# Performance work log

Measured on AMD Instinct MI355X. Metric: run time of the kernel, lower is better.

## Reference

```python
import jax, jax.numpy as jnp
import numpy as np

B, T, V = 128, 400, 148
E, ENC, DEC, NM, A, H = 512, 512, 1024, 80, 128, 256

def conv1d(x, w, pad):
    # x: [B,C_in,L], w: [C_out,C_in,K]
    return jax.lax.conv_general_dilated(x, w, (1,), [(pad, pad)],
                                        dimension_numbers=('NCH', 'OIH', 'NCH'))

def setup_inputs() -> dict:
    key = jax.random.key(0)
    ks = jax.random.split(key, 40)
    rn = lambda k, shp, s: jax.random.normal(k, shp, jnp.float32) * s
    inp = {
        'text': jax.random.randint(ks[0], (B, T), 0, V, jnp.int32),
        'mels': rn(ks[1], (B, NM, T), 1.0),
        'emb': rn(ks[2], (V, E), 0.3),
        'enc_conv_w': rn(ks[3], (ENC, E, 5), 0.02), 'enc_conv_b': jnp.zeros((ENC,)),
        'bn_g': jnp.ones((ENC,)), 'bn_b': jnp.zeros((ENC,)),
        'lstm_Wih': rn(ks[4], (3, 2, 4 * H, ENC), 0.04),
        'lstm_Whh': rn(ks[5], (3, 2, 4 * H, H), 0.06),
        'lstm_b': jnp.zeros((3, 2, 4 * H)),
        'pre_W1': rn(ks[6], (256, NM), 0.1), 'pre_b1': jnp.zeros((256,)),
        'pre_W2': rn(ks[7], (256, 256), 0.06), 'pre_b2': jnp.zeros((256,)),
        'att_Wq': rn(ks[8], (A, DEC), 0.03), 'att_Wm': rn(ks[9], (A, ENC), 0.04),
        'att_Wloc': rn(ks[10], (A, 2, 31), 0.1), 'att_v': rn(ks[11], (A,), 1.0),
        'dec_Wih': rn(ks[12], (4 * DEC, 256 + ENC), 0.03),
        'dec_Whh': rn(ks[13], (4 * DEC, DEC), 0.03),
        'dec_b': jnp.zeros((4 * DEC,)),
        'out_W': rn(ks[14], (NM * 3, DEC + ENC), 0.025), 'out_b': jnp.zeros((NM * 3,)),
        'post_w1': rn(ks[15], (512, NM, 5), 0.05), 'post_b1': jnp.zeros((512,)),
        'post_g': jnp.ones((512,)), 'post_bta': jnp.zeros((512,)),
        'post_w2': rn(ks[16], (NM, 512, 5), 0.02), 'post_b2': jnp.zeros((NM,)),
    }
    return inp

def reference(text, mels, emb, enc_conv_w, enc_conv_b, bn_g, bn_b,
              lstm_Wih, lstm_Whh, lstm_b, pre_W1, pre_b1, pre_W2, pre_b2,
              att_Wq, att_Wm, att_Wloc, att_v, dec_Wih, dec_Whh, dec_b,
              out_W, out_b, post_w1, post_b1, post_g, post_bta, post_w2, post_b2):
    b, t = text.shape
    n_mels = mels.shape[1]
    # --- encoder ---
    x = emb[text].transpose(0, 2, 1)                        # [B,E,T]
    x = jax.nn.relu(conv1d(x, enc_conv_w, 2) + enc_conv_b[None, :, None])
    mu = x.mean(axis=(0, 2), keepdims=True)
    var = x.var(axis=(0, 2), keepdims=True)                 # BatchNorm1d, train mode
    x = (x - mu) / jnp.sqrt(var + 1e-5) * bn_g[None, :, None] + bn_b[None, :, None]
    h = x.transpose(2, 0, 1)                                # [T,B,ENC] time-major

    def lstm_scan(seq, Wih, Whh, bb, rev):
        def step(carry, xt):
            hh, cc = carry
            g = xt @ Wih.T + hh @ Whh.T + bb
            i, f, gg, o = jnp.split(g, 4, axis=-1)
            cc = jax.nn.sigmoid(f) * cc + jax.nn.sigmoid(i) * jnp.tanh(gg)
            hh = jax.nn.sigmoid(o) * jnp.tanh(cc)
            return (hh, cc), hh
        z = jnp.zeros((seq.shape[1], Whh.shape[-1]), seq.dtype)
        _, hs = jax.lax.scan(step, (z, z), seq, reverse=rev)
        return hs

    for l in range(3):                                      # 3-layer biLSTM
        fwd = lstm_scan(h, lstm_Wih[l, 0], lstm_Whh[l, 0], lstm_b[l, 0], False)
        bwd = lstm_scan(h, lstm_Wih[l, 1], lstm_Whh[l, 1], lstm_b[l, 1], True)
        h = jnp.concatenate([fwd, bwd], axis=-1)            # [T,B,ENC]
    memory = h.transpose(1, 0, 2)                           # [B,T,ENC]
    pm = memory @ att_Wm.T                                  # [B,T,A] (constant over steps)
    mels_tm = mels.transpose(2, 0, 1)                       # [T,B,NM] teacher forcing
    D = dec_Whh.shape[-1]

    def dec_step(carry, mel_t):
        dec_in, hd, cd, cum = carry                         # cum: [B,2,T]
        pre = jax.nn.relu(jax.nn.relu(dec_in @ pre_W1.T + pre_b1) @ pre_W2.T + pre_b2)
        pl = conv1d(cum, att_Wloc, 15)                      # [B,A,T]
        pq = hd @ att_Wq.T                                  # [B,A]
        e = jnp.tanh(pq[:, None, :] + pm + pl.transpose(0, 2, 1)) @ att_v  # [B,T]
        align = jax.nn.softmax(e, axis=-1)
        ctx = jnp.einsum('bt,btd->bd', align, memory)       # [B,ENC]
        cum = cum + align[:, None, :]
        g = jnp.concatenate([pre, ctx], -1) @ dec_Wih.T + hd @ dec_Whh.T + dec_b
        i, f, gg, o = jnp.split(g, 4, axis=-1)
        cd = jax.nn.sigmoid(f) * cd + jax.nn.sigmoid(i) * jnp.tanh(gg)
        hd = jax.nn.sigmoid(o) * jnp.tanh(cd)
        mo = (jnp.concatenate([hd, ctx], -1) @ out_W.T + out_b).reshape(-1, 3, n_mels)
        gate = jax.nn.sigmoid(mo[:, :, -1])                 # [B,3]
        return (mel_t, hd, cd, cum), (mo, gate)

    dt = mels.dtype
    carry0 = (jnp.zeros((b, n_mels), dt), jnp.zeros((b, D), dt),
              jnp.zeros((b, D), dt), jnp.zeros((b, 2, t), dt))
    _, (mos, gates) = jax.lax.scan(dec_step, carry0, mels_tm)
    mel_outputs = mos.transpose(1, 0, 2, 3).reshape(b, 3 * t, n_mels).transpose(0, 2, 1)  # [B,NM,3T]
    gate_outputs = gates.transpose(1, 0, 2).reshape(b, 3 * t)
    # --- postnet ---
    p = conv1d(mel_outputs, post_w1, 2) + post_b1[None, :, None]
    mu = p.mean(axis=(0, 2), keepdims=True)
    var = p.var(axis=(0, 2), keepdims=True)
    p = (p - mu) / jnp.sqrt(var + 1e-5) * post_g[None, :, None] + post_bta[None, :, None]
    p = conv1d(jnp.tanh(p), post_w2, 2) + post_b2[None, :, None]
    mel_postnet = p + mel_outputs
    return mel_outputs, mel_postnet, gate_outputs
```

## Files before the change

### kernel.cpp

```cpp
#include <hip/hip_runtime.h>
#include <hip/hip_fp16.h>
#include <cstdio>
#include <cstddef>

typedef unsigned short u16;
typedef unsigned int u32;

#define BB   128
#define TT   400
#define EE   512
#define HH   256
#define NMEL 80
#define AA   128
#define DD   1024
#define T3   1200
#define PRESPLIT 352

__device__ __forceinline__ float b2f(u16 h) { return __uint_as_float(((u32)h) << 16); }
__device__ __forceinline__ u16 f2b(float f) {
    u32 x = __float_as_uint(f);
    u32 r = (x + 0x7FFFu + ((x >> 16) & 1u)) >> 16;
    return (u16)r;
}
__device__ __forceinline__ float sigm(float x) { return 1.0f / (1.0f + __expf(-x)); }

template<int F32> __device__ __forceinline__ float ldf(const void* p, size_t i) {
    if (F32) return ((const float*)p)[i];
    return b2f(((const u16*)p)[i]);
}
template<int F32> __device__ __forceinline__ float4 ldf4(const void* p, size_t i) {
    if (F32) return *(const float4*)((const float*)p + i);
    ushort4 w = *(const ushort4*)((const u16*)p + i);
    return make_float4(b2f(w.x), b2f(w.y), b2f(w.z), b2f(w.w));
}
template<int F32> __device__ __forceinline__ void stf(void* p, size_t i, float v) {
    if (F32) ((float*)p)[i] = v;
    else ((u16*)p)[i] = f2b(v);
}

__global__ __launch_bounds__(256) void k_detect(const void* emb, int* flag) {
    int tid = threadIdx.x;
    const u16* p = (const u16*)emb;
    int insane = 0;
    for (int i = tid; i < 4096; i += 256) {
        u16 h = p[2 * i];
        u32 ex = (h >> 7) & 0xFF;
        if (ex < 96 || ex > 159) insane++;
    }
    __shared__ int red[256];
    red[tid] = insane; __syncthreads();
    for (int st = 128; st > 0; st >>= 1) {
        if (tid < st) red[tid] += red[tid + st];
        __syncthreads();
    }
    if (tid == 0) *flag = (red[0] > 1024) ? 1 : 0;
}

template<int F32> __device__ __forceinline__ void embed_body(const int* text, const void* emb, float* X) {
    int e = blockIdx.x, b = blockIdx.y;
    for (int t = threadIdx.x; t < TT; t += 256) {
        int v = text[b * TT + t];
        X[((size_t)b * EE + e) * TT + t] = ldf<F32>(emb, (size_t)v * EE + e);
    }
}
__global__ __launch_bounds__(256) void k_embed(const int* text, const void* emb, float* X, const int* flag) {
    if (*flag) embed_body<1>(text, emb, X); else embed_body<0>(text, emb, X);
}

template<int F32> __device__ __forceinline__
void encconv_body(const float* X, const void* W, const void* bias, float* Y, float* xs) {
    int t0 = blockIdx.x * 64, o0 = blockIdx.y * 32, b = blockIdx.z;
    int tid = threadIdx.x;
    int ol = tid >> 3, tg = tid & 7;
    int o = o0 + ol, tl = tg * 8;
    float acc[8];
    float bv = ldf<F32>(bias, o);
    #pragma unroll
    for (int j = 0; j < 8; ++j) acc[j] = bv;
    for (int q = 0; q < 4; ++q) {
        __syncthreads();
        for (int idx = tid; idx < 128 * 68; idx += 256) {
            int il = idx / 68, rest = idx - il * 68;
            int t = t0 - 2 + rest;
            float v = 0.f;
            if (t >= 0 && t < TT) v = X[((size_t)b * EE + q * 128 + il) * TT + t];
            xs[idx] = v;
        }
        __syncthreads();
        size_t wbase = ((size_t)o * EE + q * 128) * 5;
        for (int il = 0; il < 128; ++il) {
            float xv[12];
            #pragma unroll
            for (int j = 0; j < 12; ++j) xv[j] = xs[il * 68 + tl + j];
            #pragma unroll
            for (int k = 0; k < 5; ++k) {
                float w = ldf<F32>(W, wbase + il * 5 + k);
                #pragma unroll
                for (int j = 0; j < 8; ++j) acc[j] += w * xv[j + k];
            }
        }
    }
    #pragma unroll
    for (int j = 0; j < 8; ++j) {
        int t = t0 + tl + j;
        if (t < TT) Y[((size_t)b * EE + o) * TT + t] = acc[j] > 0.f ? acc[j] : 0.f;
    }
}
__global__ __launch_bounds__(256) void k_encconv(const float* X, const void* W, const void* bias, float* Y, const int* flag) {
    __shared__ float xs[128 * 68];
    if (*flag) encconv_body<1>(X, W, bias, Y, xs); else encconv_body<0>(X, W, bias, Y, xs);
}

template<int INF32> __device__ __forceinline__
void bnstats_body(const void* Y, float* mu, float* rs, int L, int C, int Bn) {
    int o = blockIdx.x, tid = threadIdx.x;
    float s = 0.f, s2 = 0.f;
    for (int b = 0; b < Bn; ++b) {
        size_t base = ((size_t)b * C + o) * L;
        for (int t = tid; t < L; t += 256) {
            float v = INF32 ? ((const float*)Y)[base + t] : b2f(((const u16*)Y)[base + t]);
            s += v; s2 += v * v;
        }
    }
    __shared__ float r1[256], r2[256];
    r1[tid] = s; r2[tid] = s2; __syncthreads();
    for (int st = 128; st > 0; st >>= 1) {
        if (tid < st) { r1[tid] += r1[tid + st]; r2[tid] += r2[tid + st]; }
        __syncthreads();
    }
    if (tid == 0) {
        float n = (float)Bn * (float)L;
        float m = r1[0] / n;
        float var = r2[0] / n - m * m;
        mu[o] = m;
        rs[o] = 1.0f / sqrtf(var + 1e-5f);
    }
}
__global__ __launch_bounds__(256) void k_bnstats(const void* Y, float* mu, float* rs, int L, int C, int Bn, int inf32) {
    if (inf32) bnstats_body<1>(Y, mu, rs, L, C, Bn); else bnstats_body<0>(Y, mu, rs, L, C, Bn);
}

template<int F32> __device__ __forceinline__
void bnapply_body(const float* Y, const float* mu, const float* rs, const void* g, const void* beta,
                  float* H, float* tile) {
    int t0 = blockIdx.x * 64, c0 = blockIdx.y * 64, b = blockIdx.z;
    int tid = threadIdx.x;
    for (int idx = tid; idx < 64 * 64; idx += 256) {
        int cl = idx >> 6, tl = idx & 63;
        int t = t0 + tl, c = c0 + cl;
        float v = 0.f;
        if (t < TT) v = Y[((size_t)b * EE + c) * TT + t];
        tile[cl * 65 + tl] = (v - mu[c]) * rs[c] * ldf<F32>(g, c) + ldf<F32>(beta, c);
    }
    __syncthreads();
    for (int idx = tid; idx < 64 * 64; idx += 256) {
        int tl = idx >> 6, cl = idx & 63;
        int t = t0 + tl;
        if (t < TT) H[((size_t)t * BB + b) * EE + c0 + cl] = tile[cl * 65 + tl];
    }
}
__global__ __launch_bounds__(256) void k_bnapply(const float* Y, const float* mu, const float* rs,
                                                 const void* g, const void* beta, float* H, const int* flag) {
    __shared__ float tile[64 * 65];
    if (*flag) bnapply_body<1>(Y, mu, rs, g, beta, H, tile); else bnapply_body<0>(Y, mu, rs, g, beta, H, tile);
}

template<int F32> __device__ __forceinline__
void transEnc_body(const void* Wih, const void* Whh, float* WtE) {
    int ld = blockIdx.x;
    int k  = blockIdx.y;
    int u  = threadIdx.x;
    float4 w;
    if (k < 512) {
        size_t base = (size_t)ld * 1024 * 512;
        w.x = ldf<F32>(Wih, base + (size_t)(u)       * 512 + k);
        w.y = ldf<F32>(Wih, base + (size_t)(256 + u) * 512 + k);
        w.z = ldf<F32>(Wih, base + (size_t)(512 + u) * 512 + k);
        w.w = ldf<F32>(Wih, base + (size_t)(768 + u) * 512 + k);
    } else {
        size_t base = (size_t)ld * 1024 * 256;
        int kk = k - 512;
        w.x = ldf<F32>(Whh, base + (size_t)(u)       * 256 + kk);
        w.y = ldf<F32>(Whh, base + (size_t)(256 + u) * 256 + kk);
        w.z = ldf<F32>(Whh, base + (size_t)(512 + u) * 256 + kk);
        w.w = ldf<F32>(Whh, base + (size_t)(768 + u) * 256 + kk);
    }
    ((float4*)WtE)[((size_t)ld * 768 + k) * 256 + u] = w;
}
__global__ __launch_bounds__(256) void k_transEnc(const void* Wih, const void* Whh, float* WtE, const int* flag) {
    if (*flag) transEnc_body<1>(Wih, Whh, WtE); else transEnc_body<0>(Wih, Whh, WtE);
}

template<int F32> __device__ __forceinline__
void lstm2_body(const float* Hin, float* Hout, const float* WtE, const void* b_all, int layer,
                float* xsh, float* hsh) {
    int d = blockIdx.x >> 6;
    int b0 = (blockIdx.x & 63) * 2;
    int u = threadIdx.x;
    int ld = layer * 2 + d;
    size_t bB = (size_t)ld * 1024;
    float bi_ = ldf<F32>(b_all, bB + u),       bf_ = ldf<F32>(b_all, bB + 256 + u);
    float bg_ = ldf<F32>(b_all, bB + 512 + u), bo_ = ldf<F32>(b_all, bB + 768 + u);
    const float4* W4 = (const float4*)WtE + (size_t)ld * 768 * 256 + u;
    float c0v = 0.f, c1v = 0.f;
    hsh[u] = 0.f; hsh[256 + u] = 0.f;
    for (int s = 0; s < TT; ++s) {
        int t = d ? (TT - 1 - s) : s;
        __syncthreads();
        const float* src = Hin + ((size_t)t * BB + b0) * EE;
        xsh[u] = src[u];             xsh[256 + u] = src[256 + u];
        xsh[512 + u] = src[512 + u]; xsh[768 + u] = src[768 + u];
        __syncthreads();
        float a0i = bi_, a0f = bf_, a0g = bg_, a0o = bo_;
        float a1i = bi_, a1f = bf_, a1g = bg_, a1o = bo_;
        #pragma unroll 8
        for (int k = 0; k < 512; ++k) {
            float4 w = W4[(size_t)k * 256];
            float x0 = xsh[k], x1 = xsh[512 + k];
            a0i += w.x * x0; a0f += w.y * x0; a0g += w.z * x0; a0o += w.w * x0;
            a1i += w.x * x1; a1f += w.y * x1; a1g += w.z * x1; a1o += w.w * x1;
        }
        #pragma unroll 8
        for (int k = 0; k < 256; ++k) {
            float4 w = W4[(size_t)(512 + k) * 256];
            float h0 = hsh[k], h1 = hsh[256 + k];
            a0i += w.x * h0; a0f += w.y * h0; a0g += w.z * h0; a0o += w.w * h0;
            a1i += w.x * h1; a1f += w.y * h1; a1g += w.z * h1; a1o += w.w * h1;
        }
        float i0 = sigm(a0i), f0 = sigm(a0f), g0 = tanhf(a0g), o0v = sigm(a0o);
        c0v = f0 * c0v + i0 * g0;
        float h0v = o0v * tanhf(c0v);
        float i1 = sigm(a1i), f1 = sigm(a1f), g1 = tanhf(a1g), o1v = sigm(a1o);
        c1v = f1 * c1v + i1 * g1;
        float h1v = o1v * tanhf(c1v);
        __syncthreads();
        hsh[u] = h0v; hsh[256 + u] = h1v;
        Hout[((size_t)t * BB + b0) * EE + d * HH + u]     = h0v;
        Hout[((size_t)t * BB + b0 + 1) * EE + d * HH + u] = h1v;
    }
}
__global__ __launch_bounds__(256) void k_lstm2(const float* Hin, float* Hout, const float* WtE,
                                               const void* bb, int layer, const int* flag) {
    __shared__ __align__(16) float xsh[1024];
    __shared__ __align__(16) float hsh[512];
    if (*flag) lstm2_body<1>(Hin, Hout, WtE, bb, layer, xsh, hsh);
    else       lstm2_body<0>(Hin, Hout, WtE, bb, layer, xsh, hsh);
}

template<int F32> __device__ __forceinline__
void pm_body(const float* H1, const void* Wm, float* PM, float* xsh) {
    int t0 = blockIdx.x * 8, b = blockIdx.y;
    int tid = threadIdx.x;
    for (int idx = tid; idx < 8 * 512; idx += 128) {
        int tt = idx >> 9, k = idx & 511;
        xsh[tt * 512 + k] = H1[((size_t)(t0 + tt) * BB + b) * EE + k];
    }
    __syncthreads();
    size_t wrow = (size_t)tid * 512;
    float acc[8] = {0, 0, 0, 0, 0, 0, 0, 0};
    for (int k = 0; k < 512; k += 4) {
        float4 w = ldf4<F32>(Wm, wrow + k);
        #pragma unroll
        for (int tt = 0; tt < 8; ++tt) {
            float4 x = *(const float4*)&xsh[tt * 512 + k];
            acc[tt] += w.x * x.x; acc[tt] += w.y * x.y; acc[tt] += w.z * x.z; acc[tt] += w.w * x.w;
        }
    }
    #pragma unroll
    for (int tt = 0; tt < 8; ++tt)
        PM[((size_t)(t0 + tt) * BB + b) * AA + tid] = acc[tt];
}
__global__ __launch_bounds__(128) void k_pm(const float* H1, const void* Wm, float* PM, const int* flag) {
    __shared__ __align__(16) float xsh[8 * 512];
    if (*flag) pm_body<1>(H1, Wm, PM, xsh); else pm_body<0>(H1, Wm, PM, xsh);
}

template<int F32> __device__ __forceinline__
void transPre_body(const void* W1, const void* W2, float* W1t, float* W2t) {
    int r = blockIdx.x, j = threadIdx.x;
    if (r < 80) W1t[r * 256 + j] = ldf<F32>(W1, (size_t)j * 80 + r);
    else { int k = r - 80; W2t[k * 256 + j] = ldf<F32>(W2, (size_t)j * 256 + k); }
}
__global__ __launch_bounds__(256) void k_transPre(const void* W1, const void* W2, float* W1t, float* W2t, const int* flag) {
    if (*flag) transPre_body<1>(W1, W2, W1t, W2t); else transPre_body<0>(W1, W2, W1t, W2t);
}

template<int F32> __device__ __forceinline__
void prenet_all_body(const void* mels, const float* W1t, const float* W2t, const void* b1, const void* b2,
                     float* PREm, float* PREt, float* melsh, float* h1sh) {
    int t0 = blockIdx.x * 16, b = blockIdx.y;
    int tid = threadIdx.x;
    for (int idx = tid; idx < 16 * 80; idx += 256) {
        int tl = idx / 80, m = idx - tl * 80;
        int t = t0 + tl;
        melsh[tl * 80 + m] = (t == 0) ? 0.f : ldf<F32>(mels, ((size_t)b * NMEL + m) * TT + (t - 1));
    }
    __syncthreads();
    {
        int j = tid;
        float acc[16];
        float bv = ldf<F32>(b1, j);
        #pragma unroll
        for (int tl = 0; tl < 16; ++tl) acc[tl] = bv;
        for (int m = 0; m < 80; ++m) {
            float w = W1t[m * 256 + j];
            #pragma unroll
            for (int tl = 0; tl < 16; ++tl) acc[tl] += w * melsh[tl * 80 + m];
        }
        #pragma unroll
        for (int tl = 0; tl < 16; ++tl) h1sh[tl * 256 + j] = acc[tl] > 0.f ? acc[tl] : 0.f;
    }
    __syncthreads();
    {
        int j = tid;
        float acc[16];
        float bv = ldf<F32>(b2, j);
        #pragma unroll
        for (int tl = 0; tl < 16; ++tl) acc[tl] = bv;
        for (int k = 0; k < 256; ++k) {
            float w = W2t[k * 256 + j];
            #pragma unroll
            for (int tl = 0; tl < 16; ++tl) acc[tl] += w * h1sh[tl * 256 + k];
        }
        #pragma unroll
        for (int tl = 0; tl < 16; ++tl) {
            float v = acc[tl] > 0.f ? acc[tl] : 0.f;
            size_t ix = ((size_t)(t0 + tl) * BB + b) * HH + j;
            if (t0 < PRESPLIT) PREm[ix] = v;
            else               PREt[ix - (size_t)PRESPLIT * BB * HH] = v;
        }
    }
}
__global__ __launch_bounds__(256) void k_prenet_all(const void* mels, const float* W1t, const float* W2t,
                                                    const void* b1, const void* b2,
                                                    float* PREm, float* PREt, const int* flag) {
    __shared__ float melsh[16 * 80];
    __shared__ float h1sh[16 * 256];
    if (*flag) prenet_all_body<1>(mels, W1t, W2t, b1, b2, PREm, PREt, melsh, h1sh);
    else       prenet_all_body<0>(mels, W1t, W2t, b1, b2, PREm, PREt, melsh, h1sh);
}

__global__ void k_weff(const void* Wloc, float* weff, const int* flag) {
    int a = threadIdx.x;
    if (*flag) {
        for (int k = 0; k < 31; ++k)
            weff[a * 31 + k] = ldf<1>(Wloc, (size_t)(a * 2) * 31 + k) + ldf<1>(Wloc, (size_t)(a * 2 + 1) * 31 + k);
    } else {
        for (int k = 0; k < 31; ++k)
            weff[a * 31 + k] = ldf<0>(Wloc, (size_t)(a * 2) * 31 + k) + ldf<0>(Wloc, (size_t)(a * 2 + 1) * 31 + k);
    }
}

template<int F32> __device__ __forceinline__
void transW_body(const void* Wih, const void* Whh, float* Wt2) {
    int u = blockIdx.x * 256 + threadIdx.x;
    int k = blockIdx.y;
    float4 w;
    if (k < 768) {
        w.x = ldf<F32>(Wih, (size_t)(0 * 1024 + u) * 768 + k);
        w.y = ldf<F32>(Wih, (size_t)(1 * 1024 + u) * 768 + k);
        w.z = ldf<F32>(Wih, (size_t)(2 * 1024 + u) * 768 + k);
        w.w = ldf<F32>(Wih, (size_t)(3 * 1024 + u) * 768 + k);
    } else {
        int kk = k - 768;
        w.x = ldf<F32>(Whh, (size_t)(0 * 1024 + u) * 1024 + kk);
        w.y = ldf<F32>(Whh, (size_t)(1 * 1024 + u) * 1024 + kk);
        w.z = ldf<F32>(Whh, (size_t)(2 * 1024 + u) * 1024 + kk);
        w.w = ldf<F32>(Whh, (size_t)(3 * 1024 + u) * 1024 + kk);
    }
    ((float4*)Wt2)[(size_t)k * 1024 + u] = w;
}
__global__ __launch_bounds__(256) void k_transW(const void* Wih, const void* Whh, float* Wt2, const int* flag) {
    if (*flag) transW_body<1>(Wih, Whh, Wt2); else transW_body<0>(Wih, Whh, Wt2);
}

__global__ __launch_bounds__(256) void k_transOut(const void* outW, float* outWt, const int* flag) {
    int k = blockIdx.x;
    int j = threadIdx.x;
    if (j < 240) {
        float v = (*flag) ? ldf<1>(outW, (size_t)j * 1536 + k) : ldf<0>(outW, (size_t)j * 1536 + k);
        outWt[(size_t)k * 240 + j] = v;
    }
}
__global__ __launch_bounds__(128) void k_transWq(const void* Wq, float* Wqt, const int* flag) {
    int k = blockIdx.x;
    int a = threadIdx.x;
    float v = (*flag) ? ldf<1>(Wq, (size_t)a * 1024 + k) : ldf<0>(Wq, (size_t)a * 1024 + k);
    Wqt[(size_t)k * AA + a] = v;
}

template<int F32> __device__ __forceinline__
void att_body(int b, const float* hin, const float* ctxp, float* ctxc,
              const float* Wqt, const float* PM, float* cum, const float* weff,
              const void* att_v, const float* outWt, const void* outB, void* dout,
              const float* H1, int t,
              float* xsh, float* opart, float* pqsh, float* cpad, float* al, float* part, float* red)
{
    int tid = threadIdx.x;
    xsh[tid]       = hin[(size_t)b * DD + tid];
    xsh[512 + tid] = hin[(size_t)b * DD + 512 + tid];
    if (t > 0) xsh[1024 + (tid & 511)] = ctxp[(size_t)b * EE + (tid & 511)];
    for (int i = tid; i < 432; i += 512) {
        int pos = i - 15;
        cpad[i] = (pos >= 0 && pos < TT) ? cum[b * TT + pos] : 0.f;
    }
    __syncthreads();

    if (t > 0) {
        int j = -1, half = 0;
        if (tid < 240) { j = tid; half = 0; }
        else if (tid >= 256 && tid < 496) { j = tid - 256; half = 1; }
        if (j >= 0) {
            const float* wp = outWt + (half ? (size_t)768 * 240 : 0);
            const float* xp = xsh + (half ? 768 : 0);
            float a0 = 0, a1 = 0, a2 = 0, a3 = 0;
            for (int k = 0; k < 768; k += 4) {
                a0 += wp[(size_t)(k + 0) * 240 + j] * xp[k + 0];
                a1 += wp[(size_t)(k + 1) * 240 + j] * xp[k + 1];
                a2 += wp[(size_t)(k + 2) * 240 + j] * xp[k + 2];
                a3 += wp[(size_t)(k + 3) * 240 + j] * xp[k + 3];
            }
            opart[half * 240 + j] = (a0 + a1) + (a2 + a3);
        }
        __syncthreads();
        if (tid < 240) {
            float acc = ldf<F32>(outB, tid) + opart[tid] + opart[240 + tid];
            int jj = tid / 80, mm = tid - jj * 80;
            int col = 3 * (t - 1) + jj;
            stf<F32>(dout, (size_t)b * 96000 + (size_t)mm * 1200 + col, acc);
            if (mm == 79) stf<F32>(dout, (size_t)24576000 + (size_t)b * 1200 + col, sigm(acc));
        }
    }

    {
        int a = tid & 127, q = tid >> 7;
        float acc = 0.f;
        const float* wq = Wqt + a;
        int k0 = q * 256;
        for (int k = k0; k < k0 + 256; k += 4) {
            acc += wq[(size_t)(k + 0) * AA] * xsh[k + 0];
            acc += wq[(size_t)(k + 1) * AA] * xsh[k + 1];
            acc += wq[(size_t)(k + 2) * AA] * xsh[k + 2];
            acc += wq[(size_t)(k + 3) * AA] * xsh[k + 3];
        }
        pqsh[q * 128 + a] = acc;
    }
    __syncthreads();

    {
        int a = tid & 127, q = tid >> 7;
        float pqv = pqsh[a] + pqsh[128 + a] + pqsh[256 + a] + pqsh[384 + a];
        float vv = ldf<F32>(att_v, a);
        float wr[31];
        #pragma unroll
        for (int k = 0; k < 31; ++k) wr[k] = weff[a * 31 + k];
        int lane = tid & 63;
        int wid2 = (tid >> 6) & 1;
        for (int tt = q; tt < TT; tt += 4) {
            float acc = pqv + PM[((size_t)tt * BB + b) * AA + a];
            #pragma unroll
            for (int k = 0; k < 31; ++k) acc += wr[k] * cpad[tt + k];
            float fv = tanhf(acc) * vv;
            #pragma unroll
            for (int m = 1; m < 64; m <<= 1) fv += __shfl_xor(fv, m, 64);
            if (lane == 0) part[tt * 2 + wid2] = fv;
        }
    }
    __syncthreads();

    float mx = -1e30f;
    for (int tt = tid; tt < TT; tt += 512) { float v = part[2 * tt] + part[2 * tt + 1]; al[tt] = v; mx = fmaxf(mx, v); }
    red[tid] = mx; __syncthreads();
    for (int st = 256; st > 0; st >>= 1) { if (tid < st) red[tid] = fmaxf(red[tid], red[tid + st]); __syncthreads(); }
    mx = red[0]; __syncthreads();
    float s = 0.f;
    for (int tt = tid; tt < TT; tt += 512) { float v = __expf(al[tt] - mx); al[tt] = v; s += v; }
    red[tid] = s; __syncthreads();
    for (int st = 256; st > 0; st >>= 1) { if (tid < st) red[tid] += red[tid + st]; __syncthreads(); }
    float inv = 1.0f / red[0];
    __syncthreads();
    for (int tt = tid; tt < TT; tt += 512) { float v = al[tt] * inv; al[tt] = v; cum[b * TT + tt] += v; }
    __syncthreads();

    {
        int d = tid;
        float a0 = 0, a1 = 0, a2 = 0, a3 = 0;
        for (int tt = 0; tt < TT; tt += 4) {
            a0 += al[tt + 0] * H1[((size_t)(tt + 0) * BB + b) * EE + d];
            a1 += al[tt + 1] * H1[((size_t)(tt + 1) * BB + b) * EE + d];
            a2 += al[tt + 2] * H1[((size_t)(tt + 2) * BB + b) * EE + d];
            a3 += al[tt + 3] * H1[((size_t)(tt + 3) * BB + b) * EE + d];
        }
        ctxc[(size_t)b * EE + d] = (a0 + a1) + (a2 + a3);
    }
}

__device__ __forceinline__
void gemm_hd_body(int bid, const float* hin, const float* Wt2, float* gpart, float* xs) {
    int bt = bid >> 4, ut = bid & 15;
    int b0 = bt * 8, u0 = ut * 64;
    int tid = threadIdx.x;
    int u_l = tid & 63, bq = tid >> 6;
    int u = u0 + u_l;
    for (int idx = tid; idx < 1024 * 8; idx += 512) {
        int b_l = idx >> 10, kl = idx & 1023;
        xs[kl * 9 + b_l] = hin[(size_t)(b0 + b_l) * DD + kl];
    }
    __syncthreads();
    float ai = 0.f, af = 0.f, ag = 0.f, ao = 0.f;
    const float4* wp = (const float4*)Wt2 + (size_t)768 * 1024 + u;
    #pragma unroll 8
    for (int kl = 0; kl < 1024; ++kl) {
        float4 w = wp[(size_t)kl * 1024];
        float x = xs[kl * 9 + bq];
        ai += w.x * x; af += w.y * x; ag += w.z * x; ao += w.w * x;
    }
    ((float4*)gpart)[(size_t)(b0 + bq) * 1024 + u] = make_float4(ai, af, ag, ao);
}

__global__ __launch_bounds__(512) void k_att_gemm(const float* hin, const float* ctxp, float* ctxc,
                                                  const float* Wqt, const float* PM, float* cum, const float* weff,
                                                  const void* att_v, const float* outWt, const void* outB, void* dout,
                                                  const float* H1, const float* Wt2, float* gpart,
                                                  int t, const int* flag) {
    __shared__ __align__(16) float smem[9216];
    if (blockIdx.x < 128) {
        int b = blockIdx.x;
        float* xsh   = smem;
        float* opart = smem + 1536;
        float* pqsh  = smem + 2016;
        float* cpad  = smem + 2528;
        float* al    = smem + 2960;
        float* part  = smem + 3360;
        float* red   = smem + 4160;
        if (*flag) att_body<1>(b, hin, ctxp, ctxc, Wqt, PM, cum, weff, att_v, outWt, outB, dout, H1, t,
                               xsh, opart, pqsh, cpad, al, part, red);
        else       att_body<0>(b, hin, ctxp, ctxc, Wqt, PM, cum, weff, att_v, outWt, outB, dout, H1, t,
                               xsh, opart, pqsh, cpad, al, part, red);
    } else {
        gemm_hd_body(blockIdx.x - 128, hin, Wt2, gpart, smem);
    }
}

__global__ __launch_bounds__(512) void k_dec_lstm3(const float* PREm, const float* PREt,
                                                   const float* ctx, const float* Wt2, const void* bbp,
                                                   const float* gpart, float* hd_out, float* cd,
                                                   int t, const int* flag) {
    __shared__ float xs[768 * 9];
    int bt = blockIdx.x >> 4, ut = blockIdx.x & 15;
    int b0 = bt * 8, u0 = ut * 64;
    int tid = threadIdx.x;
    int u_l = tid & 63, bq = tid >> 6;
    int u = u0 + u_l, b = b0 + bq;
    int f32 = *flag;
    const float* prep = (t < PRESPLIT) ? (PREm + (size_t)t * BB * HH)
                                       : (PREt + (size_t)(t - PRESPLIT) * BB * HH);
    float ai, af, ag, ao;
    if (f32) {
        ai = ldf<1>(bbp, u);        af = ldf<1>(bbp, u + 1024);
        ag = ldf<1>(bbp, u + 2048); ao = ldf<1>(bbp, u + 3072);
    } else {
        ai = ldf<0>(bbp, u);        af = ldf<0>(bbp, u + 1024);
        ag = ldf<0>(bbp, u + 2048); ao = ldf<0>(bbp, u + 3072);
    }
    for (int idx = tid; idx < 768 * 8; idx += 512) {
        int b_l = idx / 768, kl = idx - b_l * 768;
        int bb_ = b0 + b_l;
        float v = (kl < 256) ? prep[(size_t)bb_ * HH + kl] : ctx[(size_t)bb_ * EE + (kl - 256)];
        xs[kl * 9 + b_l] = v;
    }
    __syncthreads();
    const float4* wp = (const float4*)Wt2 + u;
    #pragma unroll 8
    for (int kl = 0; kl < 768; ++kl) {
        float4 w = wp[(size_t)kl * 1024];
        float x = xs[kl * 9 + bq];
        ai += w.x * x; af += w.y * x; ag += w.z * x; ao += w.w * x;
    }
    float4 gp = ((const float4*)gpart)[(size_t)b * 1024 + u];
    ai += gp.x; af += gp.y; ag += gp.z; ao += gp.w;
    float iv = sigm(ai), fv = sigm(af), gv = tanhf(ag), ov = sigm(ao);
    float c = cd[(size_t)b * DD + u];
    c = fv * c + iv * gv;
    cd[(size_t)b * DD + u] = c;
    hd_out[(size_t)b * DD + u] = ov * tanhf(c);
}

template<int F32> __device__ __forceinline__
void dec_out_body(const float* hd, const float* ctx, const float* outWt, const void* outB,
                  void* dout, int t, float* xsh) {
    int b = blockIdx.x, tid = threadIdx.x;
    for (int idx = tid; idx < 1536; idx += 256)
        xsh[idx] = (idx < 1024) ? hd[(size_t)b * DD + idx] : ctx[(size_t)b * EE + (idx - 1024)];
    __syncthreads();
    if (tid < 240) {
        float a0 = 0, a1 = 0, a2 = 0, a3 = 0;
        for (int k = 0; k < 1536; k += 4) {
            a0 += outWt[(size_t)(k + 0) * 240 + tid] * xsh[k + 0];
            a1 += outWt[(size_t)(k + 1) * 240 + tid] * xsh[k + 1];
            a2 += outWt[(size_t)(k + 2) * 240 + tid] * xsh[k + 2];
            a3 += outWt[(size_t)(k + 3) * 240 + tid] * xsh[k + 3];
        }
        float acc = ldf<F32>(outB, tid) + ((a0 + a1) + (a2 + a3));
        int j = tid / 80, mm = tid - j * 80;
        int col = 3 * t + j;
        stf<F32>(dout, (size_t)b * 96000 + (size_t)mm * 1200 + col, acc);
        if (mm == 79) stf<F32>(dout, (size_t)24576000 + (size_t)b * 1200 + col, sigm(acc));
    }
}
__global__ __launch_bounds__(256) void k_dec_out2(const float* hd, const float* ctx, const float* outWt,
                                                  const void* outB, void* dout, int t, const int* flag) {
    __shared__ __align__(16) float xsh[1536];
    if (*flag) dec_out_body<1>(hd, ctx, outWt, outB, dout, t, xsh);
    else       dec_out_body<0>(hd, ctx, outWt, outB, dout, t, xsh);
}

template<int F32> __device__ __forceinline__
void post1_body(const void* dout, const void* W, const void* bias, u16* P1, u16* msh) {
    int t0 = blockIdx.x * 64, o0 = blockIdx.y * 32, b = blockIdx.z;
    int tid = threadIdx.x;
    for (int idx = tid; idx < 80 * 68; idx += 256) {
        int i = idx / 68, rest = idx - i * 68;
        int t = t0 - 2 + rest;
        u16 v = 0;
        if (t >= 0 && t < T3) v = f2b(ldf<F32>(dout, (size_t)b * 96000 + (size_t)i * 1200 + t));
        msh[idx] = v;
    }
    __syncthreads();
    int ol = tid >> 3, tg = tid & 7;
    int o = o0 + ol, tl = tg * 8;
    float acc[8];
    float bv = ldf<F32>(bias, o);
    #pragma unroll
    for (int j = 0; j < 8; ++j) acc[j] = bv;
    size_t wrow = (size_t)o * 400;
    for (int i = 0; i < 80; ++i) {
        float xv[12];
        #pragma unroll
        for (int j = 0; j < 12; ++j) xv[j] = b2f(msh[i * 68 + tl + j]);
        #pragma unroll
        for (int k = 0; k < 5; ++k) {
            float w = ldf<F32>(W, wrow + i * 5 + k);
            #pragma unroll
            for (int j = 0; j < 8; ++j) acc[j] += w * xv[j + k];
        }
    }
    #pragma unroll
    for (int j = 0; j < 8; ++j) {
        int t = t0 + tl + j;
        if (t < T3) P1[((size_t)b * EE + o) * T3 + t] = f2b(acc[j]);
    }
}
__global__ __launch_bounds__(256) void k_post1(const void* dout, const void* W, const void* bias,
                                               u16* P1, const int* flag) {
    __shared__ u16 msh[80 * 68];
    if (*flag) post1_body<1>(dout, W, bias, P1, msh); else post1_body<0>(dout, W, bias, P1, msh);
}

template<int F32> __device__ __forceinline__
void post2_body(const u16* P1, const float* mu, const float* rs, const void* g, const void* beta,
                const void* W2, const void* b2v, void* dout, float* tsh) {
    int t0 = blockIdx.x * 32, b = blockIdx.y;
    int tid = threadIdx.x;
    int tl = tid >> 3, mg = tid & 7;
    float acc[10];
    #pragma unroll
    for (int q = 0; q < 10; ++q) acc[q] = ldf<F32>(b2v, mg + 8 * q);
    for (int oc = 0; oc < 4; ++oc) {
        int o0 = oc * 128;
        __syncthreads();
        for (int idx = tid; idx < 128 * 36; idx += 256) {
            int i = idx / 36, rest = idx - i * 36;
            int t = t0 - 2 + rest;
            float v = 0.f;
            if (t >= 0 && t < T3) {
                int o = o0 + i;
                float raw = b2f(P1[((size_t)b * EE + o) * T3 + t]);
                v = tanhf((raw - mu[o]) * rs[o] * ldf<F32>(g, o) + ldf<F32>(beta, o));
            }
            tsh[i * 37 + rest] = v;
        }
        __syncthreads();
        for (int i = 0; i < 128; ++i) {
            float xv[5];
            #pragma unroll
            for (int k = 0; k < 5; ++k) xv[k] = tsh[i * 37 + tl + k];
            #pragma unroll
            for (int q = 0; q < 10; ++q) {
                int m = mg + 8 * q;
                size_t wp = ((size_t)m * 512 + o0 + i) * 5;
                acc[q] += ldf<F32>(W2, wp + 0) * xv[0];
                acc[q] += ldf<F32>(W2, wp + 1) * xv[1];
                acc[q] += ldf<F32>(W2, wp + 2) * xv[2];
                acc[q] += ldf<F32>(W2, wp + 3) * xv[3];
                acc[q] += ldf<F32>(W2, wp + 4) * xv[4];
            }
        }
    }
    int t = t0 + tl;
    if (t < T3) {
        #pragma unroll
        for (int q = 0; q < 10; ++q) {
            int m = mg + 8 * q;
            size_t idx = (size_t)b * 96000 + (size_t)m * 1200 + t;
            float res = ldf<F32>(dout, idx);
            stf<F32>(dout, (size_t)12288000 + idx, acc[q] + res);
        }
    }
}
__global__ __launch_bounds__(256) void k_post2(const u16* P1, const float* mu, const float* rs,
                                               const void* g, const void* beta, const void* W2,
                                               const void* b2v, void* dout, const int* flag) {
    __shared__ float tsh[128 * 37];
    if (*flag) post2_body<1>(P1, mu, rs, g, beta, W2, b2v, dout, tsh);
    else       post2_body<0>(P1, mu, rs, g, beta, W2, b2v, dout, tsh);
}

extern "C" void kernel_launch(void* const* d_in, const int* in_sizes, int n_in,
                              void* d_out, int out_size, void* d_ws, size_t ws_size,
                              hipStream_t stream) {
    const int*  text       = (const int*)d_in[0];
    const void* mels       = d_in[1];
    const void* emb        = d_in[2];
    const void* enc_conv_w = d_in[3];
    const void* enc_conv_b = d_in[4];
    const void* bn_g       = d_in[5];
    const void* bn_b       = d_in[6];
    const void* lstm_Wih   = d_in[7];
    const void* lstm_Whh   = d_in[8];
    const void* lstm_b     = d_in[9];
    const void* pre_W1     = d_in[10];
    const void* pre_b1     = d_in[11];
    const void* pre_W2     = d_in[12];
    const void* pre_b2     = d_in[13];
    const void* att_Wq     = d_in[14];
    const void* att_Wm     = d_in[15];
    const void* att_Wloc   = d_in[16];
    const void* att_v      = d_in[17];
    const void* dec_Wih    = d_in[18];
    const void* dec_Whh    = d_in[19];
    const void* dec_b      = d_in[20];
    const void* out_W      = d_in[21];
    const void* out_b      = d_in[22];
    const void* post_w1    = d_in[23];
    const void* post_b1    = d_in[24];
    const void* post_g     = d_in[25];
    const void* post_bta   = d_in[26];
    const void* post_w2    = d_in[27];
    const void* post_b2    = d_in[28];

    const size_t WS_NEED = 212049924;
    if (ws_size < WS_NEED) {
        fprintf(stderr, "kernel_launch: ws_size %zu < needed %zu\n", ws_size, WS_NEED);
        return;
    }
    char* ws = (char*)d_ws;
    float* X    = (float*)(ws + 0);
    float* Yf   = (float*)(ws + 104857600);
    float* H0f  = (float*)(ws + 0);
    float* Af   = (float*)(ws + 104857600);
    float* Bf   = (float*)(ws + 0);
    float* H1f  = (float*)(ws + 104857600);
    float* PM    = (float*)(ws + 0);
    float* Wt2   = (float*)(ws + 26214400);
    float* outWt = (float*)(ws + 55574528);
    float* Wqt   = (float*)(ws + 57049088);
    float* W1t   = (float*)(ws + 57573376);
    float* W2t   = (float*)(ws + 57655296);
    float* PREm  = (float*)(ws + 57917440);
    float* PREt  = (float*)d_out + 12288000;
    float* gpart = (float*)d_out + 14000000;
    u16*   P1    = (u16*)(ws + 0);
    float* WtE   = (float*)d_out;
    char* SM = ws + 209715200;
    float* weff  = (float*)(SM + 0);
    float* encmu = (float*)(SM + 16384);
    float* encrs = (float*)(SM + 18432);
    float* pmu   = (float*)(SM + 20480);
    float* prs   = (float*)(SM + 22528);
    float* cum   = (float*)(SM + 24576);
    float* ctx0  = (float*)(SM + 229376);
    float* ctx1  = (float*)(SM + 491520);
    float* hd0   = (float*)(SM + 753664);
    float* hd1   = (float*)(SM + 1277952);
    float* cd    = (float*)(SM + 1802240);
    int*   flag  = (int*)(SM + 2326528);

    k_detect<<<1, 256, 0, stream>>>(emb, flag);
    hipMemsetAsync(SM, 0, 2326528, stream);
    k_weff<<<1, 128, 0, stream>>>(att_Wloc, weff, flag);
    k_transEnc<<<dim3(6, 768), 256, 0, stream>>>(lstm_Wih, lstm_Whh, WtE, flag);

    k_embed<<<dim3(512, 128), 256, 0, stream>>>(text, emb, X, flag);
    k_encconv<<<dim3(7, 16, 128), 256, 0, stream>>>(X, enc_conv_w, enc_conv_b, Yf, flag);
    k_bnstats<<<512, 256, 0, stream>>>(Yf, encmu, encrs, 400, 512, 128, 1);
    k_bnapply<<<dim3(7, 8, 128), 256, 0, stream>>>(Yf, encmu, encrs, bn_g, bn_b, H0f, flag);
    k_lstm2<<<128, 256, 0, stream>>>(H0f, Af, WtE, lstm_b, 0, flag);
    k_lstm2<<<128, 256, 0, stream>>>(Af, Bf, WtE, lstm_b, 1, flag);
    k_lstm2<<<128, 256, 0, stream>>>(Bf, H1f, WtE, lstm_b, 2, flag);

    k_transW<<<dim3(4, 1792), 256, 0, stream>>>(dec_Wih, dec_Whh, Wt2, flag);
    k_transOut<<<1536, 256, 0, stream>>>(out_W, outWt, flag);
    k_transWq<<<1024, 128, 0, stream>>>(att_Wq, Wqt, flag);
    k_transPre<<<336, 256, 0, stream>>>(pre_W1, pre_W2, W1t, W2t, flag);
    k_pm<<<dim3(50, 128), 128, 0, stream>>>(H1f, att_Wm, PM, flag);
    k_prenet_all<<<dim3(25, 128), 256, 0, stream>>>(mels, W1t, W2t, pre_b1, pre_b2, PREm, PREt, flag);

    for (int t = 0; t < TT; ++t) {
        float* hin  = (t & 1) ? hd1 : hd0;
        float* hout = (t & 1) ? hd0 : hd1;
        float* ctxp = (t & 1) ? ctx0 : ctx1;
        float* ctxc = (t & 1) ? ctx1 : ctx0;
        k_att_gemm<<<384, 512, 0, stream>>>(hin, ctxp, ctxc, Wqt, PM, cum, weff, att_v,
                                            outWt, out_b, d_out, H1f, Wt2, gpart, t, flag);
        k_dec_lstm3<<<256, 512, 0, stream>>>(PREm, PREt, ctxc, Wt2, dec_b, gpart, hout, cd, t, flag);
    }
    k_dec_out2<<<128, 256, 0, stream>>>(hd0, ctx1, outWt, out_b, d_out, TT - 1, flag);

    k_post1<<<dim3(19, 16, 128), 256, 0, stream>>>(d_out, post_w1, post_b1, P1, flag);
    k_bnstats<<<512, 256, 0, stream>>>(P1, pmu, prs, 1200, 512, 128, 0);
    k_post2<<<dim3(38, 128), 256, 0, stream>>>(P1, pmu, prs, post_g, post_bta, post_w2, post_b2, d_out, flag);
}
```

Baseline: 141.5 ms.

## Retile decoder LSTM GEMMs to 64-batch x 16-unit blocks with k-slabs

```diff
diff --git a/kernel.cpp b/kernel.cpp
--- a/kernel.cpp
+++ b/kernel.cpp
@@ -497,25 +497,34 @@
 
 __device__ __forceinline__
 void gemm_hd_body(int bid, const float* hin, const float* Wt2, float* gpart, float* xs) {
-    int bt = bid >> 4, ut = bid & 15;
-    int b0 = bt * 8, u0 = ut * 64;
-    int tid = threadIdx.x;
-    int u_l = tid & 63, bq = tid >> 6;
+    int bt = bid >> 6, ut = bid & 63;
+    int b0 = bt * 64, u0 = ut * 16;
+    int tid = threadIdx.x;
+    int u_l = tid & 15, bl = tid >> 4;
     int u = u0 + u_l;
-    for (int idx = tid; idx < 1024 * 8; idx += 512) {
-        int b_l = idx >> 10, kl = idx & 1023;
-        xs[kl * 9 + b_l] = hin[(size_t)(b0 + b_l) * DD + kl];
-    }
-    __syncthreads();
-    float ai = 0.f, af = 0.f, ag = 0.f, ao = 0.f;
-    const float4* wp = (const float4*)Wt2 + (size_t)768 * 1024 + u;
-    #pragma unroll 8
-    for (int kl = 0; kl < 1024; ++kl) {
-        float4 w = wp[(size_t)kl * 1024];
-        float x = xs[kl * 9 + bq];
-        ai += w.x * x; af += w.y * x; ag += w.z * x; ao += w.w * x;
-    }
-    ((float4*)gpart)[(size_t)(b0 + bq) * 1024 + u] = make_float4(ai, af, ag, ao);
+    int b_a = 2 * bl, b_b = 2 * bl + 1;
+    float ai0 = 0, af0 = 0, ag0 = 0, ao0 = 0;
+    float ai1 = 0, af1 = 0, ag1 = 0, ao1 = 0;
+    for (int slab = 0; slab < 8; ++slab) {
+        int k0 = slab * 128;
+        __syncthreads();
+        for (int idx = tid; idx < 8192; idx += 512) {
+            int b_l = idx >> 7, kk = idx & 127;
+            xs[kk * 65 + b_l] = hin[(size_t)(b0 + b_l) * DD + k0 + kk];
+        }
+        __syncthreads();
+        const float4* wp = (const float4*)Wt2 + (size_t)(768 + k0) * 1024 + u;
+        #pragma unroll 4
+        for (int kk = 0; kk < 128; ++kk) {
+            float4 w = wp[(size_t)kk * 1024];
+            float x0 = xs[kk * 65 + b_a];
+            float x1 = xs[kk * 65 + b_b];
+            ai0 += w.x * x0; af0 += w.y * x0; ag0 += w.z * x0; ao0 += w.w * x0;
+            ai1 += w.x * x1; af1 += w.y * x1; ag1 += w.z * x1; ao1 += w.w * x1;
+        }
+    }
+    ((float4*)gpart)[(size_t)(b0 + b_a) * 1024 + u] = make_float4(ai0, af0, ag0, ao0);
+    ((float4*)gpart)[(size_t)(b0 + b_b) * 1024 + u] = make_float4(ai1, af1, ag1, ao1);
 }
 
 __global__ __launch_bounds__(512) void k_att_gemm(const float* hin, const float* ctxp, float* ctxc,
@@ -523,7 +532,7 @@
                                                   const void* att_v, const float* outWt, const void* outB, void* dout,
                                                   const float* H1, const float* Wt2, float* gpart,
                                                   int t, const int* flag) {
-    __shared__ __align__(16) float smem[9216];
+    __shared__ __align__(16) float smem[128 * 65];
     if (blockIdx.x < 128) {
         int b = blockIdx.x;
         float* xsh   = smem;
@@ -546,44 +555,65 @@
                                                    const float* ctx, const float* Wt2, const void* bbp,
                                                    const float* gpart, float* hd_out, float* cd,
                                                    int t, const int* flag) {
-    __shared__ float xs[768 * 9];
-    int bt = blockIdx.x >> 4, ut = blockIdx.x & 15;
-    int b0 = bt * 8, u0 = ut * 64;
-    int tid = threadIdx.x;
-    int u_l = tid & 63, bq = tid >> 6;
-    int u = u0 + u_l, b = b0 + bq;
+    __shared__ __align__(16) float xs[128 * 65];
+    int bt = blockIdx.x >> 6, ut = blockIdx.x & 63;
+    int b0 = bt * 64, u0 = ut * 16;
+    int tid = threadIdx.x;
+    int u_l = tid & 15, bl = tid >> 4;
+    int u = u0 + u_l;
+    int b_a = b0 + 2 * bl, b_b = b0 + 2 * bl + 1;
     int f32 = *flag;
     const float* prep = (t < PRESPLIT) ? (PREm + (size_t)t * BB * HH)
                                        : (PREt + (size_t)(t - PRESPLIT) * BB * HH);
-    float ai, af, ag, ao;
+    float bi, bf_, bg, bo;
     if (f32) {
-        ai = ldf<1>(bbp, u);        af = ldf<1>(bbp, u + 1024);
-        ag = ldf<1>(bbp, u + 2048); ao = ldf<1>(bbp, u + 3072);
+        bi = ldf<1>(bbp, u);        bf_ = ldf<1>(bbp, u + 1024);
+        bg = ldf<1>(bbp, u + 2048); bo  = ldf<1>(bbp, u + 3072);
     } else {
-        ai = ldf<0>(bbp, u);        af = ldf<0>(bbp, u + 1024);
-        ag = ldf<0>(bbp, u + 2048); ao = ldf<0>(bbp, u + 3072);
-    }
-    for (int idx = tid; idx < 768 * 8; idx += 512) {
-        int b_l = idx / 768, kl = idx - b_l * 768;
-        int bb_ = b0 + b_l;
-        float v = (kl < 256) ? prep[(size_t)bb_ * HH + kl] : ctx[(size_t)bb_ * EE + (kl - 256)];
-        xs[kl * 9 + b_l] = v;
-    }
-    __syncthreads();
-    const float4* wp = (const float4*)Wt2 + u;
-    #pragma unroll 8
-    for (int kl = 0; kl < 768; ++kl) {
-        float4 w = wp[(size_t)kl * 1024];
-        float x = xs[kl * 9 + bq];
-        ai += w.x * x; af += w.y * x; ag += w.z * x; ao += w.w * x;
-    }
-    float4 gp = ((const float4*)gpart)[(size_t)b * 1024 + u];
-    ai += gp.x; af += gp.y; ag += gp.z; ao += gp.w;
-    float iv = sigm(ai), fv = sigm(af), gv = tanhf(ag), ov = sigm(ao);
-    float c = cd[(size_t)b * DD + u];
-    c = fv * c + iv * gv;
-    cd[(size_t)b * DD + u] = c;
-    hd_out[(size_t)b * DD + u] = ov * tanhf(c);
+        bi = ldf<0>(bbp, u);        bf_ = ldf<0>(bbp, u + 1024);
+        bg = ldf<0>(bbp, u + 2048); bo  = ldf<0>(bbp, u + 3072);
+    }
+    float ai0 = bi, af0 = bf_, ag0 = bg, ao0 = bo;
+    float ai1 = bi, af1 = bf_, ag1 = bg, ao1 = bo;
+    for (int slab = 0; slab < 6; ++slab) {
+        int k0 = slab * 128;
+        __syncthreads();
+        for (int idx = tid; idx < 8192; idx += 512) {
+            int b_l = idx >> 7, kk = idx & 127;
+            int k = k0 + kk;
+            int bb_ = b0 + b_l;
+            float v = (k < 256) ? prep[(size_t)bb_ * HH + k] : ctx[(size_t)bb_ * EE + (k - 256)];
+            xs[kk * 65 + b_l] = v;
+        }
+        __syncthreads();
+        const float4* wp = (const float4*)Wt2 + (size_t)k0 * 1024 + u;
+        #pragma unroll 4
+        for (int kk = 0; kk < 128; ++kk) {
+            float4 w = wp[(size_t)kk * 1024];
+            float x0 = xs[kk * 65 + 2 * bl];
+            float x1 = xs[kk * 65 + 2 * bl + 1];
+            ai0 += w.x * x0; af0 += w.y * x0; ag0 += w.z * x0; ao0 += w.w * x0;
+            ai1 += w.x * x1; af1 += w.y * x1; ag1 += w.z * x1; ao1 += w.w * x1;
+        }
+    }
+    float4 gp0 = ((const float4*)gpart)[(size_t)b_a * 1024 + u];
+    float4 gp1 = ((const float4*)gpart)[(size_t)b_b * 1024 + u];
+    ai0 += gp0.x; af0 += gp0.y; ag0 += gp0.z; ao0 += gp0.w;
+    ai1 += gp1.x; af1 += gp1.y; ag1 += gp1.z; ao1 += gp1.w;
+    {
+        float iv = sigm(ai0), fv = sigm(af0), gv = tanhf(ag0), ov = sigm(ao0);
+        float c = cd[(size_t)b_a * DD + u];
+        c = fv * c + iv * gv;
+        cd[(size_t)b_a * DD + u] = c;
+        hd_out[(size_t)b_a * DD + u] = ov * tanhf(c);
+    }
+    {
+        float iv = sigm(ai1), fv = sigm(af1), gv = tanhf(ag1), ov = sigm(ao1);
+        float c = cd[(size_t)b_b * DD + u];
+        c = fv * c + iv * gv;
+        cd[(size_t)b_b * DD + u] = c;
+        hd_out[(size_t)b_b * DD + u] = ov * tanhf(c);
+    }
 }
 
 template<int F32> __device__ __forceinline__
@@ -811,9 +841,9 @@
         float* hout = (t & 1) ? hd0 : hd1;
         float* ctxp = (t & 1) ? ctx0 : ctx1;
         float* ctxc = (t & 1) ? ctx1 : ctx0;
-        k_att_gemm<<<384, 512, 0, stream>>>(hin, ctxp, ctxc, Wqt, PM, cum, weff, att_v,
+        k_att_gemm<<<256, 512, 0, stream>>>(hin, ctxp, ctxc, Wqt, PM, cum, weff, att_v,
                                             outWt, out_b, d_out, H1f, Wt2, gpart, t, flag);
-        k_dec_lstm3<<<256, 512, 0, stream>>>(PREm, PREt, ctxc, Wt2, dec_b, gpart, hout, cd, t, flag);
+        k_dec_lstm3<<<128, 512, 0, stream>>>(PREm, PREt, ctxc, Wt2, dec_b, gpart, hout, cd, t, flag);
     }
     k_dec_out2<<<128, 256, 0, stream>>>(hd0, ctx1, outWt, out_b, d_out, TT - 1, flag);
 
```

Measured after the change: 158.2 ms. 1.12x slower.
